# Kernel tuning notes

Hardware: AMD Instinct MI355X
Metric: run time of the kernel (lower is better)

## Reference

```python
import jax, jax.numpy as jnp
import numpy as np

B, G, NB, NC = 2048, 13, 5, 20  # batch, grid, anchors, classes
LAMBDA_COORD, LAMBDA_NOOBJ = 5.0, 0.5
# standard YOLOv2 anchors (grid-cell units); module's *416/32 then /grid_size cancels
ANCHORS = np.array([1.3221, 1.73145, 3.19275, 4.00944, 5.05587, 8.09892, 9.47112, 4.84053, 11.2364, 10.0071], dtype=np.float32)


def setup_inputs() -> dict:
    key = jax.random.key(0)
    k1, k2, k3, k4 = jax.random.split(key, 4)
    det = jax.random.normal(k1, (B, 125, G, G), dtype=jnp.float32)
    g = jax.random.uniform(k2, (B, NB, 25, G, G), dtype=jnp.float32)
    obj = (jax.random.uniform(k3, (B, NB, G, G)) < 0.05).astype(jnp.float32)
    g = g.at[:, :, 0:4].multiply(obj[:, :, None])  # coords zero where no object
    g = g.at[:, :, 4].set(obj)
    cls_id = jax.random.randint(k4, (B, NB, G, G), 0, NC)
    onehot = jnp.moveaxis(jax.nn.one_hot(cls_id, NC, dtype=jnp.float32), -1, 2)  # [B,5,20,G,G]
    g = g.at[:, :, 5:25].set(onehot * obj[:, :, None])
    gt_grid = g.reshape(B, 125, G, G)
    return {
        'detection_result': det,
        'gt_grid': gt_grid,
        'anchors_w': jnp.asarray(ANCHORS[0::2]),
        'anchors_h': jnp.asarray(ANCHORS[1::2]),
    }


def _masked_mean(x, m):
    s = jnp.sum(x * m)
    c = jnp.sum(m)
    return jnp.where(c > 0, s / jnp.maximum(c, 1.0), 0.0)


def _loss(det, gt, aw, ah):
    det5 = det.reshape(B, NB, 25, G, G)
    gt5 = gt.reshape(B, NB, 25, G, G)
    # per-anchor prior-scaled w/h: prior_w[k] = det[:,2] * anchor_w[k]
    px = det[:, 0][:, None]
    py = det[:, 1][:, None]
    pw = det[:, 2][:, None] * aw[None, :, None, None]  # [B,5,G,G]
    ph = det[:, 3][:, None] * ah[None, :, None, None]
    gx, gy = gt5[:, 0:1, 0], gt5[:, 0:1, 1]       # grid channels 0..3 of first slot
    gw, gh = gt5[:, 0:1, 2], gt5[:, 0:1, 3]
    # IoU exactly as compute_iou (treats (x, y, w*a, h*a) as corner coords, +1 areas)
    x1 = jnp.maximum(px, gx); y1 = jnp.maximum(py, gy)
    x2 = jnp.minimum(pw, gw); y2 = jnp.minimum(ph, gh)
    inter = (x2 - x1 + 1.0) * (y2 - y1 + 1.0)
    a1 = (pw - px + 1.0) * (ph - py + 1.0)
    a2 = (gw - gx + 1.0) * (gh - gy + 1.0)
    iou = inter / (a1 + a2 - inter)               # [B,5,G,G]
    # max_iou in the source is never updated (stays 0): conf_k *= max(iou_k, 0)
    conf = det5[:, :, 4] * jnp.where(iou >= 0.0, iou, 0.0)
    det5 = det5.at[:, :, 4].set(conf)
    obj = (gt5[:, :, 4] == 1.0).astype(det.dtype)  # [B,5,G,G]
    sq = (det5 - gt5) ** 2                         # [B,5,25,G,G]
    coord = sum(_masked_mean(sq[:, :, c], obj) for c in range(4))
    obj_loss = LAMBDA_COORD * coord + _masked_mean(sq[:, :, 4], obj)
    no_obj_loss = LAMBDA_NOOBJ * _masked_mean(sq[:, :, 4], 1.0 - obj)
    confidence = sum(_masked_mean(sq[:, k, 5:25], obj[:, k][:, None]) for k in range(NB))
    loss = obj_loss + no_obj_loss + confidence
    return loss, obj_loss, no_obj_loss, confidence


def reference(detection_result, gt_grid, anchors_w, anchors_h):
    return _loss(detection_result, gt_grid, anchors_w, anchors_h)
```

## Files before the change

kernel.cpp:

```cpp
#include <hip/hip_runtime.h>

#define NB_IMG   2048
#define GSQ      169
#define NCELLS   (NB_IMG * GSQ)
#define NANCH    5
#define ANCH_FLOATS  (25 * GSQ)
#define BATCH_FLOATS (125 * GSQ)
#define CLS_FLOATS   (20 * GSQ)
#define REC_SLOTS 16
#define PART_BYTES ((size_t)NB_IMG * REC_SLOTS * sizeof(double))


template<bool ATOMIC>
__global__ __launch_bounds__(256) void detloss_main(
    const float* __restrict__ det,
    const float* __restrict__ gt,
    const float* __restrict__ aw,
    const float* __restrict__ ah,
    double* __restrict__ ws)
{
    __shared__ unsigned long long mbits[NANCH][3];
    __shared__ float red[4][8];

    const int b    = blockIdx.x;
    const int tid  = threadIdx.x;
    const int wave = tid >> 6;
    const int lane = tid & 63;
    const size_t bbase = (size_t)b * BATCH_FLOATS;

    float Scoord = 0.f, S4 = 0.f, S5 = 0.f;
    float Scls[NANCH] = {0.f, 0.f, 0.f, 0.f, 0.f};

    if (tid < GSQ) {
        const float* dbase = det + bbase + tid;
        const float* gbase = gt  + bbase + tid;

        const float px = dbase[0 * GSQ];
        const float py = dbase[1 * GSQ];
        const float dw = dbase[2 * GSQ];
        const float dh = dbase[3 * GSQ];
        const float gx = gbase[0 * GSQ];
        const float gy = gbase[1 * GSQ];
        const float gw = gbase[2 * GSQ];
        const float gh = gbase[3 * GSQ];
        const float a2 = (gw - gx + 1.0f) * (gh - gy + 1.0f);

        #pragma unroll
        for (int k = 0; k < NANCH; ++k) {
            const float* dk = dbase + k * ANCH_FLOATS;
            const float* gk = gbase + k * ANCH_FLOATS;

            const float g4v = gk[4 * GSQ];
            const float d4v = dk[4 * GSQ];
            const bool  obj = (g4v == 1.0f);

            const float pw = dw * aw[k];
            const float ph = dh * ah[k];
            const float x1 = fmaxf(px, gx);
            const float y1 = fmaxf(py, gy);
            const float x2 = fminf(pw, gw);
            const float y2 = fminf(ph, gh);
            const float inter = (x2 - x1 + 1.0f) * (y2 - y1 + 1.0f);
            const float a1    = (pw - px + 1.0f) * (ph - py + 1.0f);
            const float iou   = inter / (a1 + a2 - inter);

            const float conf = d4v * (iou >= 0.0f ? iou : 0.0f);
            const float d4   = conf - g4v;
            const float d4sq = d4 * d4;

            S4 += obj ? d4sq : 0.0f;
            S5 += obj ? 0.0f : d4sq;

            if (k == 0) {
                if (obj) {
                    float dd;
                    dd = px - gx; Scoord += dd * dd;
                    dd = py - gy; Scoord += dd * dd;
                    dd = dw - gw; Scoord += dd * dd;
                    dd = dh - gh; Scoord += dd * dd;
                }
            } else {
                if (obj) {
                    float dd;
                    dd = dk[0 * GSQ] - gk[0 * GSQ]; Scoord += dd * dd;
                    dd = dk[1 * GSQ] - gk[1 * GSQ]; Scoord += dd * dd;
                    dd = dk[2 * GSQ] - gk[2 * GSQ]; Scoord += dd * dd;
                    dd = dk[3 * GSQ] - gk[3 * GSQ]; Scoord += dd * dd;
                }
            }

            const unsigned long long bb = __ballot(obj);
            if (lane == 0) mbits[k][wave] = bb;
        }
    }
    __syncthreads();

    const float4* dt4 = (const float4*)det;
    const float4* gt4 = (const float4*)gt;

    #pragma unroll 1
    for (int a = 0; a < NANCH; ++a) {
        const unsigned long long w0  = mbits[a][0];
        const unsigned long long w1  = mbits[a][1];
        const unsigned long long w2e = mbits[a][2] | (w0 << 41);
        if ((w0 | w1 | w2e) == 0ull) continue;

        const size_t s    = bbase + (size_t)a * ANCH_FLOATS + 5 * GSQ;
        const int    off  = (int)(s & 3);
        const size_t base4 = s >> 2;
        const int    n4   = off ? 846 : 845;

        int r0    = 4 * tid - off;
        int cell0 = r0 % GSQ; if (cell0 < 0) cell0 += GSQ;
        float accl = 0.f;

        #pragma unroll 1
        for (int i = tid; i < n4; i += 256, r0 += 1024) {
            const int wsel = cell0 >> 6;
            const int sh   = cell0 & 63;
            const unsigned long long lo = (wsel == 0) ? w0 : ((wsel == 1) ? w1 : w2e);
            const unsigned long long hi = (wsel == 0) ? w1 : w2e;
            const unsigned nib =
                (unsigned)((lo >> sh) | ((hi << 1) << (63 - sh))) & 0xFu;

            unsigned bnd;
            if ((unsigned)r0 <= 3376u) {
                bnd = 0xFu;
            } else {
                bnd  = ((unsigned)(r0 + 0) < (unsigned)CLS_FLOATS ? 1u : 0u);
                bnd |= ((unsigned)(r0 + 1) < (unsigned)CLS_FLOATS ? 2u : 0u);
                bnd |= ((unsigned)(r0 + 2) < (unsigned)CLS_FLOATS ? 4u : 0u);
                bnd |= ((unsigned)(r0 + 3) < (unsigned)CLS_FLOATS ? 8u : 0u);
            }
            const unsigned mask4 = nib & bnd;

            if (mask4) {
                const float4 dv = dt4[base4 + i];
                const float4 gv = gt4[base4 + i];
                const float de[4] = {dv.x, dv.y, dv.z, dv.w};
                const float ge[4] = {gv.x, gv.y, gv.z, gv.w};
                #pragma unroll
                for (int e = 0; e < 4; ++e) {
                    if (mask4 & (1u << e)) {
                        const float dd = de[e] - ge[e];
                        accl += dd * dd;
                    }
                }
            }
            cell0 += 10;
            if (cell0 >= GSQ) cell0 -= GSQ;
        }
        Scls[a] = accl;
    }

    float vals[8] = {Scoord, S4, S5,
                     Scls[0], Scls[1], Scls[2], Scls[3], Scls[4]};
    #pragma unroll
    for (int i = 0; i < 8; ++i) {
        #pragma unroll
        for (int off2 = 32; off2 > 0; off2 >>= 1)
            vals[i] += __shfl_down(vals[i], off2, 64);
    }

    if (lane == 0) {
        #pragma unroll
        for (int i = 0; i < 8; ++i) red[wave][i] = vals[i];
    }
    __syncthreads();

    if (tid < 13) {
        double s;
        if (tid < 8) {
            s = (double)red[0][tid] + (double)red[1][tid] +
                (double)red[2][tid] + (double)red[3][tid];
        } else {
            const int k = tid - 8;
            s = (double)(__popcll(mbits[k][0]) + __popcll(mbits[k][1]) +
                         __popcll(mbits[k][2]));
        }
        if (ATOMIC) atomicAdd(&ws[tid], s);
        else        ws[(size_t)b * REC_SLOTS + tid] = s;
    }
}

__device__ __forceinline__ void write_outputs(const double* a, float* out)
{
    const double cnt = a[8] + a[9] + a[10] + a[11] + a[12];
    const double coord = (cnt > 0.0) ? a[0] / cnt : 0.0;
    const double s4    = (cnt > 0.0) ? a[1] / cnt : 0.0;
    const double obj_loss = 5.0 * coord + s4;

    const double cntno  = (double)NCELLS * (double)NANCH - cnt;
    const double no_obj = (cntno > 0.0) ? 0.5 * a[2] / cntno : 0.0;

    double confsum = 0.0;
    for (int k = 0; k < NANCH; ++k) {
        const double ck = a[8 + k];
        if (ck > 0.0) confsum += a[3 + k] / ck;
    }
    const double loss = obj_loss + no_obj + confsum;
    out[0] = (float)loss;
    out[1] = (float)obj_loss;
    out[2] = (float)no_obj;
    out[3] = (float)confsum;
}

__global__ __launch_bounds__(256) void detloss_reduce(
    const double* __restrict__ ws, float* __restrict__ out)
{
    double loc[13];
    #pragma unroll
    for (int i = 0; i < 13; ++i) loc[i] = 0.0;

    for (int rec = threadIdx.x; rec < NB_IMG; rec += 256) {
        const double* p = ws + (size_t)rec * REC_SLOTS;
        #pragma unroll
        for (int i = 0; i < 13; ++i) loc[i] += p[i];
    }

    #pragma unroll
    for (int i = 0; i < 13; ++i) {
        #pragma unroll
        for (int off = 32; off > 0; off >>= 1)
            loc[i] += __shfl_down(loc[i], off, 64);
    }

    __shared__ double red[4][13];
    const int wave = threadIdx.x >> 6;
    const int lane = threadIdx.x & 63;
    if (lane == 0) {
        #pragma unroll
        for (int i = 0; i < 13; ++i) red[wave][i] = loc[i];
    }
    __syncthreads();

    if (threadIdx.x == 0) {
        double a[13];
        #pragma unroll
        for (int i = 0; i < 13; ++i)
            a[i] = red[0][i] + red[1][i] + red[2][i] + red[3][i];
        write_outputs(a, out);
    }
}

__global__ void detloss_final(const double* __restrict__ acc, float* __restrict__ out)
{
    if (threadIdx.x == 0 && blockIdx.x == 0) {
        double a[13];
        for (int i = 0; i < 13; ++i) a[i] = acc[i];
        write_outputs(a, out);
    }
}

extern "C" void kernel_launch(void* const* d_in, const int* in_sizes, int n_in,
                              void* d_out, int out_size, void* d_ws, size_t ws_size,
                              hipStream_t stream)
{
    const float* det = (const float*)d_in[0];
    const float* gt  = (const float*)d_in[1];
    const float* aw  = (const float*)d_in[2];
    const float* ah  = (const float*)d_in[3];
    double* ws  = (double*)d_ws;
    float*  out = (float*)d_out;

    if (ws_size >= PART_BYTES) {
        detloss_main<false><<<NB_IMG, 256, 0, stream>>>(det, gt, aw, ah, ws);
        detloss_reduce<<<1, 256, 0, stream>>>(ws, out);
    } else {
        hipMemsetAsync(ws, 0, 13 * sizeof(double), stream);
        detloss_main<true><<<NB_IMG, 256, 0, stream>>>(det, gt, aw, ah, ws);
        detloss_final<<<1, 64, 0, stream>>>(ws, out);
    }
}
```

Before: 58.09 us.

## Compact active class-loss float4 work items into shared list before loading

Replaces the per-anchor strided loop over class channels, which issued divergent masked float4 loads, with a two-phase scheme. Each thread first computes object masks for all five anchors, then a block-wide prefix scan packs only the float4 chunks that hold object cells into a shared-memory work list. Threads then walk the compacted list two entries at a time, issuing dense loads with branch-free accumulation. This cuts idle lanes and divergence in the sparse gather, at the cost of extra shared memory, a scan and an additional barrier.

```diff
diff --git a/kernel.cpp b/kernel.cpp
--- a/kernel.cpp
+++ b/kernel.cpp
@@ -9,6 +9,7 @@
 #define CLS_FLOATS   (20 * GSQ)
 #define REC_SLOTS 16
 #define PART_BYTES ((size_t)NB_IMG * REC_SLOTS * sizeof(double))
+#define LIST_CAP  4744
 
 
 template<bool ATOMIC>
@@ -20,6 +21,8 @@
     double* __restrict__ ws)
 {
     __shared__ unsigned long long mbits[NANCH][3];
+    __shared__ unsigned list[LIST_CAP];
+    __shared__ int wtot[4];
     __shared__ float red[4][8];
 
     const int b    = blockIdx.x;
@@ -29,7 +32,6 @@
     const size_t bbase = (size_t)b * BATCH_FLOATS;
 
     float Scoord = 0.f, S4 = 0.f, S5 = 0.f;
-    float Scls[NANCH] = {0.f, 0.f, 0.f, 0.f, 0.f};
 
     if (tid < GSQ) {
         const float* dbase = det + bbase + tid;
@@ -95,66 +97,130 @@
     }
     __syncthreads();
 
-    const float4* dt4 = (const float4*)det;
-    const float4* gt4 = (const float4*)gt;
-
-    #pragma unroll 1
+    unsigned pmask[NANCH];
+    int cnt = 0;
+    #pragma unroll
     for (int a = 0; a < NANCH; ++a) {
         const unsigned long long w0  = mbits[a][0];
         const unsigned long long w1  = mbits[a][1];
         const unsigned long long w2e = mbits[a][2] | (w0 << 41);
-        if ((w0 | w1 | w2e) == 0ull) continue;
-
-        const size_t s    = bbase + (size_t)a * ANCH_FLOATS + 5 * GSQ;
-        const int    off  = (int)(s & 3);
-        const size_t base4 = s >> 2;
-        const int    n4   = off ? 846 : 845;
-
-        int r0    = 4 * tid - off;
-        int cell0 = r0 % GSQ; if (cell0 < 0) cell0 += GSQ;
-        float accl = 0.f;
-
-        #pragma unroll 1
-        for (int i = tid; i < n4; i += 256, r0 += 1024) {
-            const int wsel = cell0 >> 6;
-            const int sh   = cell0 & 63;
-            const unsigned long long lo = (wsel == 0) ? w0 : ((wsel == 1) ? w1 : w2e);
-            const unsigned long long hi = (wsel == 0) ? w1 : w2e;
-            const unsigned nib =
-                (unsigned)((lo >> sh) | ((hi << 1) << (63 - sh))) & 0xFu;
-
-            unsigned bnd;
-            if ((unsigned)r0 <= 3376u) {
-                bnd = 0xFu;
-            } else {
-                bnd  = ((unsigned)(r0 + 0) < (unsigned)CLS_FLOATS ? 1u : 0u);
-                bnd |= ((unsigned)(r0 + 1) < (unsigned)CLS_FLOATS ? 2u : 0u);
-                bnd |= ((unsigned)(r0 + 2) < (unsigned)CLS_FLOATS ? 4u : 0u);
-                bnd |= ((unsigned)(r0 + 3) < (unsigned)CLS_FLOATS ? 8u : 0u);
+        const int off = (b + a + 1) & 3;
+        const int n4  = off ? 846 : 845;
+
+        int r0   = 4 * tid - off;
+        int cell = r0 % GSQ; if (cell < 0) cell += GSQ;
+        unsigned pm = 0;
+        #pragma unroll
+        for (int t = 0; t < 4; ++t) {
+            const int i = tid + 256 * t;
+            unsigned mask4 = 0;
+            if (i < n4) {
+                const int wsel = cell >> 6;
+                const int sh   = cell & 63;
+                const unsigned long long lo = (wsel == 0) ? w0 : ((wsel == 1) ? w1 : w2e);
+                const unsigned long long hi = (wsel == 0) ? w1 : w2e;
+                const unsigned nib =
+                    (unsigned)((lo >> sh) | ((hi << 1) << (63 - sh))) & 0xFu;
+                unsigned bnd;
+                if ((unsigned)r0 <= 3376u) {
+                    bnd = 0xFu;
+                } else {
+                    bnd  = ((unsigned)(r0 + 0) < (unsigned)CLS_FLOATS ? 1u : 0u);
+                    bnd |= ((unsigned)(r0 + 1) < (unsigned)CLS_FLOATS ? 2u : 0u);
+                    bnd |= ((unsigned)(r0 + 2) < (unsigned)CLS_FLOATS ? 4u : 0u);
+                    bnd |= ((unsigned)(r0 + 3) < (unsigned)CLS_FLOATS ? 8u : 0u);
+                }
+                mask4 = nib & bnd;
             }
-            const unsigned mask4 = nib & bnd;
-
-            if (mask4) {
-                const float4 dv = dt4[base4 + i];
-                const float4 gv = gt4[base4 + i];
-                const float de[4] = {dv.x, dv.y, dv.z, dv.w};
-                const float ge[4] = {gv.x, gv.y, gv.z, gv.w};
-                #pragma unroll
-                for (int e = 0; e < 4; ++e) {
-                    if (mask4 & (1u << e)) {
-                        const float dd = de[e] - ge[e];
-                        accl += dd * dd;
-                    }
-                }
+            pm  |= mask4 << (4 * t);
+            cnt += (mask4 != 0u) ? 1 : 0;
+            r0  += 1024;
+            cell += 10; if (cell >= GSQ) cell -= GSQ;
+        }
+        pmask[a] = pm;
+    }
+
+    int scan = cnt;
+    #pragma unroll
+    for (int d = 1; d < 64; d <<= 1) {
+        const int v = __shfl_up(scan, d, 64);
+        scan += (lane >= d) ? v : 0;
+    }
+    if (lane == 63) wtot[wave] = scan;
+    __syncthreads();
+    int wbase = 0;
+    #pragma unroll
+    for (int wv = 0; wv < 4; ++wv) wbase += (wv < wave) ? wtot[wv] : 0;
+    const int total = wtot[0] + wtot[1] + wtot[2] + wtot[3];
+    int pos = wbase + scan - cnt;
+
+    #pragma unroll
+    for (int a = 0; a < NANCH; ++a) {
+        #pragma unroll
+        for (int t = 0; t < 4; ++t) {
+            const unsigned m4 = (pmask[a] >> (4 * t)) & 0xFu;
+            if (m4) {
+                list[pos] = ((unsigned)a << 14) | (m4 << 10) | (unsigned)(tid + 256 * t);
+                ++pos;
             }
-            cell0 += 10;
-            if (cell0 >= GSQ) cell0 -= GSQ;
-        }
-        Scls[a] = accl;
-    }
-
-    float vals[8] = {Scoord, S4, S5,
-                     Scls[0], Scls[1], Scls[2], Scls[3], Scls[4]};
+        }
+    }
+    const int totalPad = (total + 511) & ~511;
+    for (int p = total + tid; p < totalPad; p += 256) list[p] = 0u;
+    __syncthreads();
+
+    const float4* dt4 = (const float4*)det;
+    const float4* gt4 = (const float4*)gt;
+    const unsigned bb32 = (unsigned)(b * BATCH_FLOATS);
+
+    float Sc0 = 0.f, Sc1 = 0.f, Sc2 = 0.f, Sc3 = 0.f, Sc4 = 0.f;
+
+    #pragma unroll 1
+    for (int w = tid; w < totalPad; w += 512) {
+        const unsigned eA = list[w];
+        const unsigned eB = list[w + 256];
+
+        const unsigned iA = eA & 1023u, mA = (eA >> 10) & 0xFu, aA = eA >> 14;
+        const unsigned iB = eB & 1023u, mB = (eB >> 10) & 0xFu, aB = eB >> 14;
+        const size_t b4A = (size_t)((bb32 + aA * (unsigned)ANCH_FLOATS + 5u * GSQ) >> 2) + iA;
+        const size_t b4B = (size_t)((bb32 + aB * (unsigned)ANCH_FLOATS + 5u * GSQ) >> 2) + iB;
+
+        const float4 dvA = dt4[b4A];
+        const float4 gvA = gt4[b4A];
+        const float4 dvB = dt4[b4B];
+        const float4 gvB = gt4[b4B];
+
+        {
+            const float d0 = dvA.x - gvA.x, d1 = dvA.y - gvA.y,
+                        d2 = dvA.z - gvA.z, d3 = dvA.w - gvA.w;
+            const float v0 = (mA & 1u) ? d0 * d0 : 0.f;
+            const float v1 = (mA & 2u) ? d1 * d1 : 0.f;
+            const float v2 = (mA & 4u) ? d2 * d2 : 0.f;
+            const float v3 = (mA & 8u) ? d3 * d3 : 0.f;
+            const float sv = (v0 + v1) + (v2 + v3);
+            Sc0 += (aA == 0u) ? sv : 0.f;
+            Sc1 += (aA == 1u) ? sv : 0.f;
+            Sc2 += (aA == 2u) ? sv : 0.f;
+            Sc3 += (aA == 3u) ? sv : 0.f;
+            Sc4 += (aA == 4u) ? sv : 0.f;
+        }
+        {
+            const float d0 = dvB.x - gvB.x, d1 = dvB.y - gvB.y,
+                        d2 = dvB.z - gvB.z, d3 = dvB.w - gvB.w;
+            const float v0 = (mB & 1u) ? d0 * d0 : 0.f;
+            const float v1 = (mB & 2u) ? d1 * d1 : 0.f;
+            const float v2 = (mB & 4u) ? d2 * d2 : 0.f;
+            const float v3 = (mB & 8u) ? d3 * d3 : 0.f;
+            const float sv = (v0 + v1) + (v2 + v3);
+            Sc0 += (aB == 0u) ? sv : 0.f;
+            Sc1 += (aB == 1u) ? sv : 0.f;
+            Sc2 += (aB == 2u) ? sv : 0.f;
+            Sc3 += (aB == 3u) ? sv : 0.f;
+            Sc4 += (aB == 4u) ? sv : 0.f;
+        }
+    }
+
+    float vals[8] = {Scoord, S4, S5, Sc0, Sc1, Sc2, Sc3, Sc4};
     #pragma unroll
     for (int i = 0; i < 8; ++i) {
         #pragma unroll
```

New measurement: 61.48 us. +5.8%, slower.
